# Performance work log

Hardware: AMD Instinct MI355X
Metric: run time of the kernel (lower is better)

Reference implementation:

```python
import jax, jax.numpy as jnp
import numpy as np

NPOINT = 1024   # samples (farthest point sampling count)
RADIUS = 0.2    # ball query radius
K = 32          # neighbors per ball


def farthest_point_sample(xyz, npoint):
    # xyz: [B, N, 3] -> idx: [B, npoint] int32
    B, N, _ = xyz.shape
    def body(carry, _):
        dists, farthest = carry                      # [B,N], [B]
        centroid = jnp.take_along_axis(xyz, farthest[:, None, None], axis=1)  # [B,1,3]
        d = jnp.sum((xyz - centroid) ** 2, axis=-1)  # [B,N]
        dists = jnp.minimum(dists, d)
        nxt = jnp.argmax(dists, axis=-1).astype(jnp.int32)
        return (dists, nxt), farthest
    init = (jnp.full((B, N), 1e10, dtype=xyz.dtype), jnp.zeros((B,), jnp.int32))
    _, idx = jax.lax.scan(body, init, None, length=npoint)
    return jnp.transpose(idx)  # [B, npoint]


def query_ball_point(radius, k, xyz, new_xyz):
    # returns idx: [B, S, k] int32 -- first k in-radius point indices,
    # padded with the first found index (TF query_ball_point semantics)
    N = xyz.shape[1]
    sqd = jnp.sum((new_xyz[:, :, None, :] - xyz[:, None, :, :]) ** 2, axis=-1)  # [B,S,N]
    cand = jnp.where(sqd <= radius * radius, jnp.arange(N, dtype=jnp.int32)[None, None, :], N)
    idx = jnp.sort(cand, axis=-1)[..., :k]          # [B,S,k]
    first = idx[..., :1]
    return jnp.where(idx == N, first, idx).astype(jnp.int32)


def group_point(x, idx):
    # x: [B,N,C], idx: [B,S,k] -> [B,S,k,C]
    return jax.vmap(lambda xb, ib: xb[ib])(x, idx)


def setup_inputs() -> dict:
    key = jax.random.key(0)
    ks = jax.random.split(key, 8)
    B, N, C = 16, 4096, 64
    xyz = jax.random.uniform(ks[0], (B, N, 3), dtype=jnp.float32)
    points = jax.random.normal(ks[1], (B, N, C), dtype=jnp.float32)
    cin = 3 + C  # use_xyz concat
    widths = [64, 64, 128]
    W, b, c = [], [], cin
    for i, w in enumerate(widths):
        W.append(jax.random.normal(ks[2 + i], (c, w), dtype=jnp.float32) * (1.0 / np.sqrt(c)))
        b.append(jnp.zeros((w,), dtype=jnp.float32))
        c = w
    return {"xyz": xyz, "points": points,
            "W0": W[0], "b0": b[0], "W1": W[1], "b1": b[1], "W2": W[2], "b2": b[2]}


def reference(xyz, points, W0, b0, W1, b1, W2, b2):
    # --- sample_and_group ---
    fps_idx = farthest_point_sample(xyz, NPOINT)                 # [B,S]
    new_xyz = jax.vmap(lambda xb, ib: xb[ib])(xyz, fps_idx)      # [B,S,3]
    idx = query_ball_point(RADIUS, K, xyz, new_xyz)              # [B,S,K]
    grouped_xyz = group_point(xyz, idx) - new_xyz[:, :, None, :] # [B,S,K,3]
    grouped_points = group_point(points, idx)                    # [B,S,K,C]
    new_points = jnp.concatenate([grouped_xyz, grouped_points], axis=-1)  # [B,S,K,3+C]
    # --- shared 1x1-conv MLP (bn=False, relu) ---
    for W, bb in ((W0, b0), (W1, b1), (W2, b2)):
        new_points = jax.nn.relu(jnp.einsum('bskc,cd->bskd', new_points, W) + bb)
    # --- max pool over neighborhood ---
    new_points = jnp.max(new_points, axis=2)                     # [B,S,Cout]
    return new_xyz, new_points, idx
```

## Files before the change

kernel.cpp:

```cpp
#include <hip/hip_runtime.h>

#define BB 16
#define NN 4096
#define SS 1024
#define KNB 32
#define FPT 16
#define FNW 4

typedef unsigned long long ull;
typedef float v2f __attribute__((ext_vector_type(2)));

__device__ __forceinline__ float sqd3(float dx, float dy, float dz) {
    return __fadd_rn(__fadd_rn(__fmul_rn(dx, dx), __fmul_rn(dy, dy)), __fmul_rn(dz, dz));
}

#define DPPMAX(m, ctrl, rm)                                                              \
    {                                                                                    \
        unsigned _t = (unsigned)__builtin_amdgcn_update_dpp((int)(m), (int)(m), (ctrl),  \
                                                            (rm), 0xf, false);           \
        (m) = ((m) > _t) ? (m) : _t;                                                     \
    }

__global__ __launch_bounds__(256) void fused1_kernel(const float* __restrict__ xyz,
                                                     const float* __restrict__ points,
                                                     const float* __restrict__ W0,
                                                     const float* __restrict__ b0,
                                                     float* __restrict__ P1,
                                                     float4* __restrict__ xyz4,
                                                     float* __restrict__ out_newxyz) {
    __shared__ union {
        struct {
            float4 pts4[NN];
            ull    keys[2][FNW];
            int    hist[SS];
        } f;
        float w0s[67 * 64];
    } sm;

    const int t = threadIdx.x;

    if (blockIdx.x < BB) {
        const int b = blockIdx.x;
        const int lane = t & 63;
        const float* src = xyz + (size_t)b * (NN * 3) + (size_t)t * (FPT * 3);

        v2f px2[8], py2[8], pz2[8], d2[8];
        {
            float c48[48];
#pragma unroll
            for (int m = 0; m < 12; ++m) {
                float4 v = ((const float4*)src)[m];
                c48[4 * m + 0] = v.x; c48[4 * m + 1] = v.y;
                c48[4 * m + 2] = v.z; c48[4 * m + 3] = v.w;
            }
#pragma unroll
            for (int j = 0; j < 8; ++j) {
                px2[j] = (v2f){c48[6 * j + 0], c48[6 * j + 3]};
                py2[j] = (v2f){c48[6 * j + 1], c48[6 * j + 4]};
                pz2[j] = (v2f){c48[6 * j + 2], c48[6 * j + 5]};
                d2[j]  = (v2f){1e10f, 1e10f};
                sm.f.pts4[t * FPT + 2 * j + 0] = make_float4(px2[j].x, py2[j].x, pz2[j].x, 0.f);
                sm.f.pts4[t * FPT + 2 * j + 1] = make_float4(px2[j].y, py2[j].y, pz2[j].y, 0.f);
            }
        }
        __syncthreads();

        int far = 0;
        for (int it = 0; it < SS; ++it) {
            if (t == 0) sm.f.hist[it] = far;
            if (it == SS - 1) break;
            float4 c = sm.f.pts4[far];

            float bv0 = -1.f, bv1 = -1.f;
            int bn0 = 0, bn1 = 0;
            {
#pragma clang fp contract(off)
                v2f cx2 = {c.x, c.x}, cy2 = {c.y, c.y}, cz2 = {c.z, c.z};
#pragma unroll
                for (int j = 0; j < 4; ++j) {
                    v2f dx = px2[j] - cx2;
                    v2f dy = py2[j] - cy2;
                    v2f dz = pz2[j] - cz2;
                    v2f s = (dx * dx + dy * dy) + dz * dz;
                    float d0 = fminf(d2[j].x, s.x);
                    float d1 = fminf(d2[j].y, s.y);
                    d2[j] = (v2f){d0, d1};
                    bool g0 = d0 > bv0; bv0 = g0 ? d0 : bv0; bn0 = g0 ? (t * FPT + 2 * j + 0) : bn0;
                    bool g1 = d1 > bv0; bv0 = g1 ? d1 : bv0; bn0 = g1 ? (t * FPT + 2 * j + 1) : bn0;
                }
#pragma unroll
                for (int j = 4; j < 8; ++j) {
                    v2f dx = px2[j] - cx2;
                    v2f dy = py2[j] - cy2;
                    v2f dz = pz2[j] - cz2;
                    v2f s = (dx * dx + dy * dy) + dz * dz;
                    float d0 = fminf(d2[j].x, s.x);
                    float d1 = fminf(d2[j].y, s.y);
                    d2[j] = (v2f){d0, d1};
                    bool g0 = d0 > bv1; bv1 = g0 ? d0 : bv1; bn1 = g0 ? (t * FPT + 2 * j + 0) : bn1;
                    bool g1 = d1 > bv1; bv1 = g1 ? d1 : bv1; bn1 = g1 ? (t * FPT + 2 * j + 1) : bn1;
                }
            }
            bool gm = bv1 > bv0;
            float bv = gm ? bv1 : bv0;
            int bn = gm ? bn1 : bn0;

            unsigned mb = __float_as_uint(bv);
            DPPMAX(mb, 0x111, 0xf);
            DPPMAX(mb, 0x112, 0xf);
            DPPMAX(mb, 0x114, 0xf);
            DPPMAX(mb, 0x118, 0xf);
            DPPMAX(mb, 0x142, 0xa);
            DPPMAX(mb, 0x143, 0xc);
            unsigned vmb = (unsigned)__builtin_amdgcn_readlane((int)mb, 63);

            ull ball = __ballot(__float_as_uint(bv) == vmb);
            int sel = __ffsll(ball) - 1;
            int widx = __builtin_amdgcn_readlane(bn, sel);

            const int par = it & 1;
            if (lane == 0) {
                sm.f.keys[par][t >> 6] = ((ull)vmb << 32) | (unsigned)(~widx);
            }
            __syncthreads();
            ulonglong2 ka = *(const ulonglong2*)&sm.f.keys[par][0];
            ulonglong2 kb = *(const ulonglong2*)&sm.f.keys[par][2];
            ull a0 = (ka.x > ka.y) ? ka.x : ka.y;
            ull a1 = (kb.x > kb.y) ? kb.x : kb.y;
            ull best = (a0 > a1) ? a0 : a1;
            far = (int)(~(unsigned)best);
        }
        __syncthreads();
#pragma unroll
        for (int r = 0; r < 4; ++r) {
            int it2 = t + 256 * r;
            int fi = sm.f.hist[it2];
            float4 c = sm.f.pts4[fi];
            size_t o = ((size_t)b * SS + it2) * 3;
            out_newxyz[o + 0] = c.x;
            out_newxyz[o + 1] = c.y;
            out_newxyz[o + 2] = c.z;
        }
    } else {
        for (int i = t; i < 67 * 64; i += 256) sm.w0s[i] = W0[i];
        __syncthreads();
        const int lane = t & 63;
        const int wv = t >> 6;

        {
            int n0 = (blockIdx.x - BB) * 256 + t;
            xyz4[n0] = make_float4(xyz[3 * n0 + 0], xyz[3 * n0 + 1], xyz[3 * n0 + 2], 0.f);
        }

        const float bias = b0[lane];
        const int base = (blockIdx.x - BB) * 256 + wv * 64;
        for (int pi = 0; pi < 64; ++pi) {
            const int n = base + pi;
            const float* xp = xyz + (size_t)n * 3;
            const float* pp = points + (size_t)n * 64;
            float acc = bias;
            acc = fmaf(xp[0], sm.w0s[0 * 64 + lane], acc);
            acc = fmaf(xp[1], sm.w0s[1 * 64 + lane], acc);
            acc = fmaf(xp[2], sm.w0s[2 * 64 + lane], acc);
#pragma unroll 8
            for (int c = 0; c < 64; ++c) acc = fmaf(pp[c], sm.w0s[(3 + c) * 64 + lane], acc);
            P1[(size_t)n * 64 + lane] = acc;
        }
    }
}

__global__ __launch_bounds__(256) void k3_kernel(const float4* __restrict__ xyz4,
                                                 const float* __restrict__ P1,
                                                 const float* __restrict__ W0,
                                                 const float* __restrict__ W1,
                                                 const float* __restrict__ b1,
                                                 const float* __restrict__ W2,
                                                 const float* __restrict__ b2,
                                                 float* __restrict__ d_out) {
    const int t = threadIdx.x;
    const int lane = t & 63;
    const int wv = t >> 6;
    const int b = blockIdx.x >> 10;

    __shared__ int   ids[KNB];
    __shared__ int   bq[2][FNW];
    __shared__ float part[4][128];
    __shared__ float hs[4][8][64];

    float* out_newxyz = d_out;
    float* out_points = d_out + (size_t)BB * SS * 3;
    float* out_idx    = d_out + (size_t)BB * SS * 3 + (size_t)BB * SS * 128;

    const size_t q = (size_t)blockIdx.x;
    const float nx = out_newxyz[q * 3 + 0];
    const float ny = out_newxyz[q * 3 + 1];
    const float nz = out_newxyz[q * 3 + 2];

    const float qv = nx * W0[lane] + ny * W0[64 + lane] + nz * W0[128 + lane];
    float w1col[64];
#pragma unroll
    for (int i = 0; i < 64; ++i) w1col[i] = W1[i * 64 + lane];
    const float b1v = b1[lane];

    {
        const float4* xb4 = xyz4 + (size_t)b * NN;
        const float R2 = 0.04f;
        const ull ltm = (1ull << lane) - 1ull;
        int total = 0, c0 = 0, pr = 0;
        float4 pcA = xb4[t];
        float4 pcB = xb4[256 + t];
        while (true) {
            float4 curA = pcA, curB = pcB;
            int nc0 = c0 + 512;
            if (nc0 < NN) {
                pcA = xb4[nc0 + t];
                pcB = xb4[nc0 + 256 + t];
            }
            float dA = sqd3(curA.x - nx, curA.y - ny, curA.z - nz);
            float dB = sqd3(curB.x - nx, curB.y - ny, curB.z - nz);
            bool inA = (dA <= R2);
            bool inB = (dB <= R2);
            ull mA = __ballot(inA);
            ull mB = __ballot(inB);
            if (lane == 0) bq[pr][wv] = __popcll(mA) | (__popcll(mB) << 8);
            __syncthreads();
            int p0 = bq[pr][0], p1 = bq[pr][1], p2 = bq[pr][2], p3 = bq[pr][3];
            int a0 = p0 & 0xff, a1 = p1 & 0xff, a2 = p2 & 0xff, a3 = p3 & 0xff;
            int e0 = p0 >> 8, e1 = p1 >> 8, e2 = p2 >> 8, e3 = p3 >> 8;
            int sumA = a0 + a1 + a2 + a3;
            int baseA = total + (wv > 0 ? a0 : 0) + (wv > 1 ? a1 : 0) + (wv > 2 ? a2 : 0);
            int baseB = total + sumA + (wv > 0 ? e0 : 0) + (wv > 1 ? e1 : 0) + (wv > 2 ? e2 : 0);
            int posA = baseA + __popcll(mA & ltm);
            int posB = baseB + __popcll(mB & ltm);
            if (inA && posA < KNB) ids[posA] = c0 + t;
            if (inB && posB < KNB) ids[posB] = c0 + 256 + t;
            total += sumA + e0 + e1 + e2 + e3;
            c0 = nc0;
            pr ^= 1;
            if (total >= KNB || c0 >= NN) break;
        }
        __syncthreads();
        int cnt = (total < KNB) ? total : KNB;
        if (t >= cnt && t < KNB) ids[t] = ids[0];
    }
    __syncthreads();
    if (t < KNB) out_idx[q * KNB + t] = (float)ids[t];

    const float* P1b = P1 + (size_t)b * NN * 64;
#pragma unroll
    for (int kk = 0; kk < 8; ++kk) {
        int n = ids[wv * 8 + kk];
        float v = P1b[(size_t)n * 64 + lane] - qv;
        hs[wv][kk][lane] = fmaxf(v, 0.f);
    }

    float acc[8];
#pragma unroll
    for (int kk = 0; kk < 8; ++kk) acc[kk] = b1v;
#pragma unroll
    for (int qd = 0; qd < 16; ++qd) {
#pragma unroll
        for (int kk = 0; kk < 8; ++kk) {
            float4 h4 = *(const float4*)&hs[wv][kk][4 * qd];
            acc[kk] = fmaf(h4.x, w1col[4 * qd + 0], acc[kk]);
            acc[kk] = fmaf(h4.y, w1col[4 * qd + 1], acc[kk]);
            acc[kk] = fmaf(h4.z, w1col[4 * qd + 2], acc[kk]);
            acc[kk] = fmaf(h4.w, w1col[4 * qd + 3], acc[kk]);
        }
    }
#pragma unroll
    for (int kk = 0; kk < 8; ++kk) hs[wv][kk][lane] = fmaxf(acc[kk], 0.f);

    float w2a[64], w2b[64];
#pragma unroll
    for (int i = 0; i < 64; ++i) {
        w2a[i] = W2[i * 128 + lane];
        w2b[i] = W2[i * 128 + 64 + lane];
    }
    const float b2a = b2[lane];
    const float b2bv = b2[64 + lane];
    float acc3a[8], acc3b[8];
#pragma unroll
    for (int kk = 0; kk < 8; ++kk) { acc3a[kk] = b2a; acc3b[kk] = b2bv; }
#pragma unroll
    for (int qd = 0; qd < 16; ++qd) {
#pragma unroll
        for (int kk = 0; kk < 8; ++kk) {
            float4 h4 = *(const float4*)&hs[wv][kk][4 * qd];
            acc3a[kk] = fmaf(h4.x, w2a[4 * qd + 0], acc3a[kk]);
            acc3a[kk] = fmaf(h4.y, w2a[4 * qd + 1], acc3a[kk]);
            acc3a[kk] = fmaf(h4.z, w2a[4 * qd + 2], acc3a[kk]);
            acc3a[kk] = fmaf(h4.w, w2a[4 * qd + 3], acc3a[kk]);
            acc3b[kk] = fmaf(h4.x, w2b[4 * qd + 0], acc3b[kk]);
            acc3b[kk] = fmaf(h4.y, w2b[4 * qd + 1], acc3b[kk]);
            acc3b[kk] = fmaf(h4.z, w2b[4 * qd + 2], acc3b[kk]);
            acc3b[kk] = fmaf(h4.w, w2b[4 * qd + 3], acc3b[kk]);
        }
    }
    float ma = 0.f, mbv = 0.f;
#pragma unroll
    for (int kk = 0; kk < 8; ++kk) {
        ma = fmaxf(ma, acc3a[kk]);
        mbv = fmaxf(mbv, acc3b[kk]);
    }
    part[wv][lane] = ma;
    part[wv][64 + lane] = mbv;
    __syncthreads();
    if (t < 128) {
        float v = fmaxf(fmaxf(part[0][t], part[1][t]), fmaxf(part[2][t], part[3][t]));
        out_points[q * 128 + t] = v;
    }
}

extern "C" void kernel_launch(void* const* d_in, const int* in_sizes, int n_in,
                              void* d_out, int out_size, void* d_ws, size_t ws_size,
                              hipStream_t stream) {
    const float* xyz    = (const float*)d_in[0];
    const float* points = (const float*)d_in[1];
    const float* W0     = (const float*)d_in[2];
    const float* b0     = (const float*)d_in[3];
    const float* W1     = (const float*)d_in[4];
    const float* b1     = (const float*)d_in[5];
    const float* W2     = (const float*)d_in[6];
    const float* b2     = (const float*)d_in[7];
    float* out = (float*)d_out;
    float*  P1   = (float*)d_ws;
    float4* xyz4 = (float4*)((char*)d_ws + (size_t)BB * NN * 64 * 4);

    hipLaunchKernelGGL(fused1_kernel, dim3(BB + (BB * NN) / 256), dim3(256), 0, stream,
                       xyz, points, W0, b0, P1, xyz4, out);
    hipLaunchKernelGGL(k3_kernel, dim3(BB * SS), dim3(256), 0, stream,
                       xyz4, P1, W0, W1, b1, W2, b2, out);
}
```

Baseline: 776.2 us.

## Stage W2 transposed in LDS and defer W1 loads to cut register pressure

The layer-3 weights are no longer held as 128 per-lane registers. Each block stages W2 transposed into padded shared memory before the ball query, and the loop reads float4 weight rows from there. The W0/W1 register loads move to after the neighbor search, and launch bounds request 2 blocks per CU, all to lower VGPR use and raise occupancy. In exchange each block fetches and transposes the full W2 from global memory and adds about 35 KB of LDS, which may itself cap occupancy.

New measurement: 762.0 us. Within noise of the previous version (-1.8%).

```diff
diff --git a/kernel.cpp b/kernel.cpp
--- a/kernel.cpp
+++ b/kernel.cpp
@@ -169,23 +169,24 @@
     }
 }
 
-__global__ __launch_bounds__(256) void k3_kernel(const float4* __restrict__ xyz4,
-                                                 const float* __restrict__ P1,
-                                                 const float* __restrict__ W0,
-                                                 const float* __restrict__ W1,
-                                                 const float* __restrict__ b1,
-                                                 const float* __restrict__ W2,
-                                                 const float* __restrict__ b2,
-                                                 float* __restrict__ d_out) {
+__global__ __launch_bounds__(256, 2) void k3_kernel(const float4* __restrict__ xyz4,
+                                                    const float* __restrict__ P1,
+                                                    const float* __restrict__ W0,
+                                                    const float* __restrict__ W1,
+                                                    const float* __restrict__ b1,
+                                                    const float* __restrict__ W2,
+                                                    const float* __restrict__ b2,
+                                                    float* __restrict__ d_out) {
     const int t = threadIdx.x;
     const int lane = t & 63;
     const int wv = t >> 6;
     const int b = blockIdx.x >> 10;
 
+    __shared__ float w2t[128][68];
+    __shared__ float hs[4][8][64];
+    __shared__ float part[4][128];
     __shared__ int   ids[KNB];
     __shared__ int   bq[2][FNW];
-    __shared__ float part[4][128];
-    __shared__ float hs[4][8][64];
 
     float* out_newxyz = d_out;
     float* out_points = d_out + (size_t)BB * SS * 3;
@@ -196,11 +197,18 @@
     const float ny = out_newxyz[q * 3 + 1];
     const float nz = out_newxyz[q * 3 + 2];
 
-    const float qv = nx * W0[lane] + ny * W0[64 + lane] + nz * W0[128 + lane];
-    float w1col[64];
-#pragma unroll
-    for (int i = 0; i < 64; ++i) w1col[i] = W1[i * 64 + lane];
-    const float b1v = b1[lane];
+#pragma unroll
+    for (int r = 0; r < 8; ++r) {
+        int m = t + 256 * r;
+        int o = m & 127;
+        int i4 = m >> 7;
+        float4 v;
+        v.x = W2[(4 * i4 + 0) * 128 + o];
+        v.y = W2[(4 * i4 + 1) * 128 + o];
+        v.z = W2[(4 * i4 + 2) * 128 + o];
+        v.w = W2[(4 * i4 + 3) * 128 + o];
+        *(float4*)&w2t[o][4 * i4] = v;
+    }
 
     {
         const float4* xb4 = xyz4 + (size_t)b * NN;
@@ -246,6 +254,12 @@
     __syncthreads();
     if (t < KNB) out_idx[q * KNB + t] = (float)ids[t];
 
+    const float qv = nx * W0[lane] + ny * W0[64 + lane] + nz * W0[128 + lane];
+    float w1col[64];
+#pragma unroll
+    for (int i = 0; i < 64; ++i) w1col[i] = W1[i * 64 + lane];
+    const float b1v = b1[lane];
+
     const float* P1b = P1 + (size_t)b * NN * 64;
 #pragma unroll
     for (int kk = 0; kk < 8; ++kk) {
@@ -271,12 +285,6 @@
 #pragma unroll
     for (int kk = 0; kk < 8; ++kk) hs[wv][kk][lane] = fmaxf(acc[kk], 0.f);
 
-    float w2a[64], w2b[64];
-#pragma unroll
-    for (int i = 0; i < 64; ++i) {
-        w2a[i] = W2[i * 128 + lane];
-        w2b[i] = W2[i * 128 + 64 + lane];
-    }
     const float b2a = b2[lane];
     const float b2bv = b2[64 + lane];
     float acc3a[8], acc3b[8];
@@ -284,17 +292,19 @@
     for (int kk = 0; kk < 8; ++kk) { acc3a[kk] = b2a; acc3b[kk] = b2bv; }
 #pragma unroll
     for (int qd = 0; qd < 16; ++qd) {
+        float4 wa = *(const float4*)&w2t[lane][4 * qd];
+        float4 wb = *(const float4*)&w2t[64 + lane][4 * qd];
 #pragma unroll
         for (int kk = 0; kk < 8; ++kk) {
             float4 h4 = *(const float4*)&hs[wv][kk][4 * qd];
-            acc3a[kk] = fmaf(h4.x, w2a[4 * qd + 0], acc3a[kk]);
-            acc3a[kk] = fmaf(h4.y, w2a[4 * qd + 1], acc3a[kk]);
-            acc3a[kk] = fmaf(h4.z, w2a[4 * qd + 2], acc3a[kk]);
-            acc3a[kk] = fmaf(h4.w, w2a[4 * qd + 3], acc3a[kk]);
-            acc3b[kk] = fmaf(h4.x, w2b[4 * qd + 0], acc3b[kk]);
-            acc3b[kk] = fmaf(h4.y, w2b[4 * qd + 1], acc3b[kk]);
-            acc3b[kk] = fmaf(h4.z, w2b[4 * qd + 2], acc3b[kk]);
-            acc3b[kk] = fmaf(h4.w, w2b[4 * qd + 3], acc3b[kk]);
+            acc3a[kk] = fmaf(h4.x, wa.x, acc3a[kk]);
+            acc3a[kk] = fmaf(h4.y, wa.y, acc3a[kk]);
+            acc3a[kk] = fmaf(h4.z, wa.z, acc3a[kk]);
+            acc3a[kk] = fmaf(h4.w, wa.w, acc3a[kk]);
+            acc3b[kk] = fmaf(h4.x, wb.x, acc3b[kk]);
+            acc3b[kk] = fmaf(h4.y, wb.y, acc3b[kk]);
+            acc3b[kk] = fmaf(h4.z, wb.z, acc3b[kk]);
+            acc3b[kk] = fmaf(h4.w, wb.w, acc3b[kk]);
         }
     }
     float ma = 0.f, mbv = 0.f;
```
